# Kernel optimization log

Hardware: AMD Instinct MI355X
Metric: run time of the kernel (lower is better)

## Reference

```python
import jax, jax.numpy as jnp
import numpy as np

N_NODES = 100000
N_EDGES = 1600000
N_EMBED = 48
N_CONVS = 6
N_GRAPHS = 1000
VOCAB = 100


def setup_inputs() -> dict:
    key = jax.random.key(0)
    ks = jax.random.split(key, 20)
    AtomicNum = jax.random.randint(ks[0], (N_NODES,), 0, VOCAB)
    Edge = jax.random.randint(ks[1], (2, N_EDGES), 0, N_NODES)
    graph_id = jnp.sort(jax.random.randint(ks[2], (N_NODES,), 0, N_GRAPHS))
    s = 1.0 / np.sqrt(N_EMBED)
    def lin(k):
        k1, k2 = jax.random.split(k)
        w = jax.random.uniform(k1, (N_EMBED, N_EMBED), jnp.float32, -s, s)
        b = jax.random.uniform(k2, (N_EMBED,), jnp.float32, -s, s)
        return w, b
    def stacked(k):
        ws, bs = zip(*[lin(kk) for kk in jax.random.split(k, N_CONVS)])
        return jnp.stack(ws), jnp.stack(bs)
    emb = jax.random.normal(ks[3], (VOCAB, N_EMBED), jnp.float32)
    msg_w1, msg_b1 = stacked(ks[4])
    msg_w2, msg_b2 = stacked(ks[5])
    upd_w1, upd_b1 = stacked(ks[6])
    upd_w2, upd_b2 = stacked(ks[7])
    ro_w1, ro_b1 = lin(ks[8])
    k1, k2 = jax.random.split(ks[9])
    ro_w2 = jax.random.uniform(k1, (N_EMBED, 1), jnp.float32, -s, s)
    ro_b2 = jax.random.uniform(k2, (1,), jnp.float32, -s, s)
    return dict(AtomicNum=AtomicNum, Edge=Edge, graph_id=graph_id, emb=emb,
                msg_w1=msg_w1, msg_b1=msg_b1, msg_w2=msg_w2, msg_b2=msg_b2,
                upd_w1=upd_w1, upd_b1=upd_b1, upd_w2=upd_w2, upd_b2=upd_b2,
                ro_w1=ro_w1, ro_b1=ro_b1, ro_w2=ro_w2, ro_b2=ro_b2)


def reference(AtomicNum, Edge, graph_id, emb,
              msg_w1, msg_b1, msg_w2, msg_b2,
              upd_w1, upd_b1, upd_w2, upd_b2,
              ro_w1, ro_b1, ro_w2, ro_b2):
    n_nodes = AtomicNum.shape[0]
    src, dst = Edge[0], Edge[1]
    h = emb[AtomicNum]  # [N, d]
    for l in range(N_CONVS):
        # gather endpoint features, elementwise product, message MLP
        x = h[src] * h[dst]                                      # [E, d]
        m = jax.nn.relu(x @ msg_w1[l] + msg_b1[l]) @ msg_w2[l] + msg_b2[l]
        agg = jax.ops.segment_sum(m, dst, num_segments=n_nodes)  # scatter_add
        u = jax.nn.relu(agg @ upd_w1[l] + upd_b1[l]) @ upd_w2[l] + upd_b2[l]
        h = h + u  # residual update
    y = jax.nn.relu(h @ ro_w1 + ro_b1) @ ro_w2 + ro_b2           # [N, 1]
    # per-graph sum readout (== torch.split by Natom + sum per chunk)
    out = jax.ops.segment_sum(y[:, 0], graph_id, num_segments=N_GRAPHS)
    return out
```

## Files before the change

### kernel.cpp

```cpp
#include <hip/hip_runtime.h>
#include <hip/hip_bf16.h>


#define NE 48
#define NB_SH 8
#define SLDS_CAP 1024

typedef __attribute__((ext_vector_type(8))) short short8;
typedef __attribute__((ext_vector_type(4))) float floatx4;

__device__ __forceinline__ unsigned short bf16_rne(float v) {
    unsigned u = __float_as_uint(v);
    u += 0x7FFFu + ((u >> 16) & 1u);
    return (unsigned short)(u >> 16);
}

__device__ __forceinline__ void split8p(const float* __restrict__ x, short8& hi, short8& lo) {
    union { unsigned u[4]; short8 s; } H, L;
#pragma unroll
    for (int i = 0; i < 4; ++i) {
        float a = x[2 * i], b = x[2 * i + 1];
        __hip_bfloat162 h2 = __float22bfloat162_rn(make_float2(a, b));
        unsigned h = *reinterpret_cast<unsigned*>(&h2);
        float ra = a - __uint_as_float(h << 16);
        float rb = b - __uint_as_float(h & 0xFFFF0000u);
        __hip_bfloat162 l2 = __float22bfloat162_rn(make_float2(ra, rb));
        H.u[i] = h;
        L.u[i] = *reinterpret_cast<unsigned*>(&l2);
    }
    hi = H.s; lo = L.s;
}

__device__ __forceinline__ short8 cvt8(const float* __restrict__ x) {
    union { unsigned u[4]; short8 s; } H;
#pragma unroll
    for (int i = 0; i < 4; ++i) {
        __hip_bfloat162 h2 = __float22bfloat162_rn(make_float2(x[2 * i], x[2 * i + 1]));
        H.u[i] = *reinterpret_cast<unsigned*>(&h2);
    }
    return H.s;
}

__device__ __forceinline__ void gemm3(const short8& ah0, const short8& al0,
                                      const short8& ah1, const short8& al1,
                                      const short8* __restrict__ hi,
                                      const short8* __restrict__ lo,
                                      int lane, floatx4* acc) {
#pragma unroll
    for (int t = 0; t < 3; ++t) {
        short8 bh0 = hi[(t * 2 + 0) * 64 + lane];
        short8 bh1 = hi[(t * 2 + 1) * 64 + lane];
        short8 bl0 = lo[(t * 2 + 0) * 64 + lane];
        short8 bl1 = lo[(t * 2 + 1) * 64 + lane];
        floatx4 c = {0.0f, 0.0f, 0.0f, 0.0f};
        c = __builtin_amdgcn_mfma_f32_16x16x32_bf16(ah0, bh0, c, 0, 0, 0);
        c = __builtin_amdgcn_mfma_f32_16x16x32_bf16(ah1, bh1, c, 0, 0, 0);
        c = __builtin_amdgcn_mfma_f32_16x16x32_bf16(al0, bh0, c, 0, 0, 0);
        c = __builtin_amdgcn_mfma_f32_16x16x32_bf16(al1, bh1, c, 0, 0, 0);
        c = __builtin_amdgcn_mfma_f32_16x16x32_bf16(ah0, bl0, c, 0, 0, 0);
        c = __builtin_amdgcn_mfma_f32_16x16x32_bf16(ah1, bl1, c, 0, 0, 0);
        acc[t] = c;
    }
}

__global__ __launch_bounds__(256) void embed_kernel(const int* __restrict__ an,
                                                    const float* __restrict__ emb,
                                                    float* __restrict__ h, int n4) {
    int i = blockIdx.x * 256 + threadIdx.x;
    if (i >= n4) return;
    int n = i / 12, q = i - n * 12;
    ((float4*)h)[i] = ((const float4*)emb)[an[n] * 12 + q];
}

__global__ __launch_bounds__(256) void fold_kernel(const float* __restrict__ w2,
                                                   const float* __restrict__ u1,
                                                   const float* __restrict__ b2,
                                                   float* __restrict__ F,
                                                   float* __restrict__ b2u1) {
    int idx = blockIdx.x * 256 + threadIdx.x;
    if (idx < 6 * NE * NE) {
        int l = idx / (NE * NE);
        int r = idx - l * NE * NE;
        int k = r / NE, j = r - (r / NE) * NE;
        const float* wrow = w2 + (size_t)l * NE * NE + k * NE;
        const float* ucol = u1 + (size_t)l * NE * NE + j;
        float s = 0.0f;
#pragma unroll 8
        for (int q = 0; q < NE; ++q) s = fmaf(wrow[q], ucol[q * NE], s);
        F[idx] = s;
    } else if (idx < 6 * NE * NE + 6 * NE) {
        int r = idx - 6 * NE * NE;
        int l = r / NE, j = r - l * NE;
        const float* bv = b2 + (size_t)l * NE;
        const float* ucol = u1 + (size_t)l * NE * NE + j;
        float s = 0.0f;
#pragma unroll 8
        for (int q = 0; q < NE; ++q) s = fmaf(bv[q], ucol[q * NE], s);
        b2u1[r] = s;
    }
}

__global__ __launch_bounds__(256) void hist_kernel(const int* __restrict__ dst,
                                                   int* __restrict__ cnt, int E) {
    int e = blockIdx.x * 256 + threadIdx.x;
    if (e < E) atomicAdd(&cnt[dst[e]], 1);
}

__global__ __launch_bounds__(256) void scansum_kernel(const int* __restrict__ cnt,
                                                      int* __restrict__ bsum, int N) {
    __shared__ int sw[4];
    const int tid = threadIdx.x, lane = tid & 63, wid = tid >> 6;
    int base = blockIdx.x * 1024;
    int v = 0;
#pragma unroll
    for (int k = 0; k < 4; ++k) {
        int i = base + k * 256 + tid;
        v += (i < N) ? cnt[i] : 0;
    }
#pragma unroll
    for (int o = 1; o < 64; o <<= 1) v += __shfl_xor(v, o, 64);
    if (lane == 0) sw[wid] = v;
    __syncthreads();
    if (tid == 0) bsum[blockIdx.x] = sw[0] + sw[1] + sw[2] + sw[3];
}

__global__ __launch_bounds__(256) void scanb_kernel(int* __restrict__ bsum, int nblk) {
    __shared__ int s[256];
    int tid = threadIdx.x;
    s[tid] = (tid < nblk) ? bsum[tid] : 0;
    __syncthreads();
    if (tid == 0) {
        int run = 0;
        for (int i = 0; i < nblk; ++i) { int t = s[i]; s[i] = run; run += t; }
    }
    __syncthreads();
    if (tid < nblk) bsum[tid] = s[tid];
}

__global__ __launch_bounds__(1024) void scanfix_kernel(const int* __restrict__ cnt,
                                                       const int* __restrict__ bsum,
                                                       int* __restrict__ offs,
                                                       int* __restrict__ gpos, int N) {
    __shared__ int swave[16];
    const int tid = threadIdx.x, lane = tid & 63, wid = tid >> 6;
    int i = blockIdx.x * 1024 + tid;
    int orig = (i < N) ? cnt[i] : 0;
    int v = orig;
#pragma unroll
    for (int off = 1; off < 64; off <<= 1) {
        int u = __shfl_up(v, off, 64);
        if (lane >= off) v += u;
    }
    if (lane == 63) swave[wid] = v;
    __syncthreads();
    if (wid == 0) {
        int w = (lane < 16) ? swave[lane] : 0;
#pragma unroll
        for (int off = 1; off < 16; off <<= 1) {
            int u = __shfl_up(w, off, 64);
            if (lane >= off) w += u;
        }
        if (lane < 16) swave[lane] = w;
    }
    __syncthreads();
    int prefix = (wid > 0) ? swave[wid - 1] : 0;
    int val = bsum[blockIdx.x] + prefix + v - orig;
    if (i < N) {
        offs[i] = val;
        if ((i & 255) == 0) gpos[i >> 8] = val;
    }
}

__global__ __launch_bounds__(256) void partA_kernel(const int* __restrict__ src,
                                                    const int* __restrict__ dst,
                                                    int* __restrict__ gpos,
                                                    int2* __restrict__ pairbuf,
                                                    int E, int NB) {
    __shared__ int lhist[512];
    __shared__ int lbase[512];
    const int tid = threadIdx.x;
    for (int i = tid; i < NB; i += 256) lhist[i] = 0;
    __syncthreads();
    const int base = blockIdx.x * 2048;
    int ssrc[8], sdst[8], rnk[8];
#pragma unroll
    for (int k = 0; k < 8; ++k) {
        int e = base + k * 256 + tid;
        if (e < E) {
            ssrc[k] = src[e]; sdst[k] = dst[e];
            rnk[k] = atomicAdd(&lhist[sdst[k] >> NB_SH], 1);
        }
    }
    __syncthreads();
    for (int i = tid; i < NB; i += 256) {
        int c = lhist[i];
        lbase[i] = c ? atomicAdd(&gpos[i], c) : 0;
    }
    __syncthreads();
#pragma unroll
    for (int k = 0; k < 8; ++k) {
        int e = base + k * 256 + tid;
        if (e < E)
            pairbuf[lbase[sdst[k] >> NB_SH] + rnk[k]] = make_int2(ssrc[k], sdst[k]);
    }
}

__global__ __launch_bounds__(256) void partB_kernel(const int2* __restrict__ pairbuf,
                                                    int* __restrict__ offs,
                                                    int* __restrict__ colsrc, int E) {
    int e = blockIdx.x * 256 + threadIdx.x;
    if (e < E) {
        int2 p = pairbuf[e];
        int pos = atomicAdd(&offs[p.y], 1);
        colsrc[pos] = p.x;
    }
}

__global__ __launch_bounds__(256) void pack_all_kernel(const float* __restrict__ w0,
                                                       const float* __restrict__ w1m,
                                                       const float* __restrict__ w2m,
                                                       const float* __restrict__ w3m,
                                                       short8* __restrict__ hi,
                                                       short8* __restrict__ lo) {
    int idx = blockIdx.x * 256 + threadIdx.x;
    if (idx >= 3 * 2304 + 384) return;
    int slot = idx / 2304;
    int rem  = idx - slot * 2304;
    const float* w = (slot == 0) ? w0 : (slot == 1) ? w1m : (slot == 2) ? w2m : w3m;
    int lane = rem & 63;
    int s = (rem >> 6) & 1;
    int t = (rem >> 7) % 3;
    int l = (rem >> 7) / 3;
    short8 h8, l8;
#pragma unroll
    for (int i = 0; i < 8; ++i) {
        int k = s * 32 + (lane >> 4) * 8 + i;
        int j = t * 16 + (lane & 15);
        float v = (k < NE) ? w[l * NE * NE + k * NE + j] : 0.0f;
        unsigned short hh = bf16_rne(v);
        float hf = __uint_as_float((unsigned)hh << 16);
        unsigned short ll = bf16_rne(v - hf);
        h8[i] = (short)hh;
        l8[i] = (short)ll;
    }
    hi[idx] = h8;
    lo[idx] = l8;
}

__global__ __launch_bounds__(64, 4) void layer_kernel(
    const float* __restrict__ hin,
    const int* __restrict__ colsrc,
    const int* __restrict__ ends,
    const int* __restrict__ cnt,
    float* __restrict__ hout,
    const short8* __restrict__ bhi,
    const short8* __restrict__ blo,
    const float* __restrict__ b1,
    const short8* __restrict__ f1hi, const short8* __restrict__ f1lo,
    const float* __restrict__ b2u1v,
    const float* __restrict__ ub1,
    const short8* __restrict__ u2hi, const short8* __restrict__ u2lo,
    const float* __restrict__ ub2,
    int N,
    int final_layer,
    const int* __restrict__ gid,
    const short8* __restrict__ rw1hi, const short8* __restrict__ rw1lo,
    const float* __restrict__ rb1, const float* __restrict__ rw2,
    const float* __restrict__ rb2, float* __restrict__ out)
{
    __shared__ float mytile[16][52];
    __shared__ float hdls[16][48];
    __shared__ int   slds[SLDS_CAP];
    const int lane = threadIdx.x;
    const int n0   = blockIdx.x * 16;
    if (n0 >= N) return;

    const int m  = lane & 15;
    const int kb = lane >> 4;

    {
        const float4* sp = (const float4*)(hin + (size_t)n0 * NE);
        float4* dp = (float4*)hdls;
#pragma unroll
        for (int f = 0; f < 3; ++f) dp[lane + f * 64] = sp[lane + f * 64];
    }

    const int mydeg = cnt[n0 + m];
    const int myend = ends[n0 + m];

    const int beg0 = __shfl(myend - mydeg, 0, 64);
    const int endL = __shfl(myend, 15, 64);
    const int tot  = endL - beg0;
    const bool uselds = (tot <= SLDS_CAP);
    if (uselds) {
        for (int i = lane; i < tot; i += 64) slds[i] = colsrc[beg0 + i];
    }

    short8 bh[6];
#pragma unroll
    for (int i = 0; i < 6; ++i) bh[i] = bhi[i * 64 + lane];
    const float bb0 = b1[m], bb1 = b1[16 + m], bb2 = b1[32 + m];
    const float rbb0 = fmaxf(bb0, 0.0f), rbb1 = fmaxf(bb1, 0.0f), rbb2 = fmaxf(bb2, 0.0f);
    const float rbb_mine = (lane < 16) ? rbb0 : (lane < 32) ? rbb1 : rbb2;

    asm volatile("s_waitcnt vmcnt(0) lgkmcnt(0)" ::: "memory");

#pragma unroll 1
    for (int nn = 0; nn < 16; ++nn) {
        const int deg = __shfl(mydeg, nn, 64);
        const int end = __shfl(myend, nn, 64);
        const int beg = end - deg;

        const float* hr = hdls[nn];
        float4 d0a = *(const float4*)(hr + kb * 8);
        float4 d0b = *(const float4*)(hr + kb * 8 + 4);
        float4 d1a = make_float4(0, 0, 0, 0), d1b = d1a;
        if (kb < 2) {
            d1a = *(const float4*)(hr + 32 + kb * 8);
            d1b = *(const float4*)(hr + 32 + kb * 8 + 4);
        }

        float s0 = 0.0f, s1 = 0.0f, s2 = 0.0f;
        const int ntile = (deg + 15) >> 4;

        for (int it = 0; it < ntile; ++it) {
            const int rem = deg - it * 16;
            int srow;
            if (uselds) srow = (m < rem) ? slds[beg - beg0 + it * 16 + m] : N;
            else        srow = (m < rem) ? colsrc[beg + it * 16 + m] : N;
            const float* hs = hin + (size_t)srow * NE + kb * 8;

            float x0[8], x1[8];
            {
                float4 a0 = ((const float4*)hs)[0];
                float4 a1 = ((const float4*)hs)[1];
                x0[0] = a0.x * d0a.x; x0[1] = a0.y * d0a.y; x0[2] = a0.z * d0a.z; x0[3] = a0.w * d0a.w;
                x0[4] = a1.x * d0b.x; x0[5] = a1.y * d0b.y; x0[6] = a1.z * d0b.z; x0[7] = a1.w * d0b.w;
            }
            if (kb < 2) {
                float4 a0 = ((const float4*)(hs + 32))[0];
                float4 a1 = ((const float4*)(hs + 32))[1];
                x1[0] = a0.x * d1a.x; x1[1] = a0.y * d1a.y; x1[2] = a0.z * d1a.z; x1[3] = a0.w * d1a.w;
                x1[4] = a1.x * d1b.x; x1[5] = a1.y * d1b.y; x1[6] = a1.z * d1b.z; x1[7] = a1.w * d1b.w;
            } else {
#pragma unroll
                for (int i = 0; i < 8; ++i) x1[i] = 0.0f;
            }

            short8 ah0 = cvt8(x0);
            short8 ah1 = cvt8(x1);

#pragma unroll
            for (int t = 0; t < 3; ++t) {
                floatx4 cc = {0.0f, 0.0f, 0.0f, 0.0f};
                cc = __builtin_amdgcn_mfma_f32_16x16x32_bf16(ah0, bh[t * 2 + 0], cc, 0, 0, 0);
                cc = __builtin_amdgcn_mfma_f32_16x16x32_bf16(ah1, bh[t * 2 + 1], cc, 0, 0, 0);
                const float bb = (t == 0) ? bb0 : (t == 1) ? bb1 : bb2;
                float ts = 0.0f;
#pragma unroll
                for (int r = 0; r < 4; ++r)
                    ts += fmaxf(cc[r] + bb, 0.0f);
                if (t == 0) s0 += ts; else if (t == 1) s1 += ts; else s2 += ts;
            }
        }

        s0 += __shfl_xor(s0, 16, 64); s0 += __shfl_xor(s0, 32, 64);
        s1 += __shfl_xor(s1, 16, 64); s1 += __shfl_xor(s1, 32, 64);
        s2 += __shfl_xor(s2, 16, 64); s2 += __shfl_xor(s2, 32, 64);

        float t1v = __shfl(s1, lane & 15, 64);
        float t2v = __shfl(s2, lane & 15, 64);
        float val = (lane < 16) ? s0 : (lane < 32) ? t1v : t2v;
        const float npad = (float)(ntile * 16 - deg);
        val = fmaf(-npad, rbb_mine, val);
        if (lane < 48) mytile[nn][lane] = val;
    }
    asm volatile("s_waitcnt lgkmcnt(0)" ::: "memory");

    float c0[8], c1[8];
    {
        const float* row = &mytile[m][0];
        *(float4*)(c0)     = *(const float4*)(row + kb * 8);
        *(float4*)(c0 + 4) = *(const float4*)(row + kb * 8 + 4);
        if (kb < 2) {
            *(float4*)(c1)     = *(const float4*)(row + 32 + kb * 8);
            *(float4*)(c1 + 4) = *(const float4*)(row + 32 + kb * 8 + 4);
        } else {
#pragma unroll
            for (int i = 0; i < 8; ++i) c1[i] = 0.0f;
        }
    }
    asm volatile("s_waitcnt lgkmcnt(0)" ::: "memory");
    short8 ah0, al0, ah1, al1;
    split8p(c0, ah0, al0);
    split8p(c1, ah1, al1);

    floatx4 acc[3];
    gemm3(ah0, al0, ah1, al1, f1hi, f1lo, lane, acc);
    {
        float dj[3], bj[3];
#pragma unroll
        for (int t = 0; t < 3; ++t) { dj[t] = b2u1v[t * 16 + m]; bj[t] = ub1[t * 16 + m]; }
#pragma unroll
        for (int r = 0; r < 4; ++r) {
            float fd = (float)__shfl(mydeg, kb * 4 + r, 64);
#pragma unroll
            for (int t = 0; t < 3; ++t)
                acc[t][r] = fmaxf(fmaf(fd, dj[t], acc[t][r]) + bj[t], 0.0f);
        }
    }

#pragma unroll
    for (int t = 0; t < 3; ++t)
#pragma unroll
        for (int r = 0; r < 4; ++r)
            mytile[kb * 4 + r][t * 16 + m] = acc[t][r];
    asm volatile("s_waitcnt lgkmcnt(0)" ::: "memory");
    {
        const float* row = &mytile[m][0];
        *(float4*)(c0)     = *(const float4*)(row + kb * 8);
        *(float4*)(c0 + 4) = *(const float4*)(row + kb * 8 + 4);
        if (kb < 2) {
            *(float4*)(c1)     = *(const float4*)(row + 32 + kb * 8);
            *(float4*)(c1 + 4) = *(const float4*)(row + 32 + kb * 8 + 4);
        } else {
#pragma unroll
            for (int i = 0; i < 8; ++i) c1[i] = 0.0f;
        }
    }
    asm volatile("s_waitcnt lgkmcnt(0)" ::: "memory");
    split8p(c0, ah0, al0);
    split8p(c1, ah1, al1);
    gemm3(ah0, al0, ah1, al1, u2hi, u2lo, lane, acc);

    {
        float bj[3];
#pragma unroll
        for (int t = 0; t < 3; ++t) bj[t] = ub2[t * 16 + m];
#pragma unroll
        for (int r = 0; r < 4; ++r) {
#pragma unroll
            for (int t = 0; t < 3; ++t)
                acc[t][r] += hdls[kb * 4 + r][t * 16 + m] + bj[t];
        }
    }

    if (!final_layer) {
#pragma unroll
        for (int r = 0; r < 4; ++r) {
            const size_t row = (size_t)(n0 + kb * 4 + r) * NE;
#pragma unroll
            for (int t = 0; t < 3; ++t)
                hout[row + t * 16 + m] = acc[t][r];
        }
        return;
    }

#pragma unroll
    for (int t = 0; t < 3; ++t)
#pragma unroll
        for (int r = 0; r < 4; ++r)
            mytile[kb * 4 + r][t * 16 + m] = acc[t][r];
    asm volatile("s_waitcnt lgkmcnt(0)" ::: "memory");
    {
        const float* row = &mytile[m][0];
        *(float4*)(c0)     = *(const float4*)(row + kb * 8);
        *(float4*)(c0 + 4) = *(const float4*)(row + kb * 8 + 4);
        if (kb < 2) {
            *(float4*)(c1)     = *(const float4*)(row + 32 + kb * 8);
            *(float4*)(c1 + 4) = *(const float4*)(row + 32 + kb * 8 + 4);
        } else {
#pragma unroll
            for (int i = 0; i < 8; ++i) c1[i] = 0.0f;
        }
    }
    split8p(c0, ah0, al0);
    split8p(c1, ah1, al1);
    gemm3(ah0, al0, ah1, al1, rw1hi, rw1lo, lane, acc);

    float p[4] = {0.0f, 0.0f, 0.0f, 0.0f};
    {
        float bj[3], wj[3];
#pragma unroll
        for (int t = 0; t < 3; ++t) { bj[t] = rb1[t * 16 + m]; wj[t] = rw2[t * 16 + m]; }
#pragma unroll
        for (int t = 0; t < 3; ++t)
#pragma unroll
            for (int r = 0; r < 4; ++r)
                p[r] = fmaf(fmaxf(acc[t][r] + bj[t], 0.0f), wj[t], p[r]);
    }
#pragma unroll
    for (int o = 1; o < 16; o <<= 1) {
#pragma unroll
        for (int r = 0; r < 4; ++r) p[r] += __shfl_xor(p[r], o, 16);
    }
    if (m == 0) {
        float b2v = rb2[0];
#pragma unroll
        for (int r = 0; r < 4; ++r) {
            int n = n0 + kb * 4 + r;
            atomicAdd(out + gid[n], p[r] + b2v);
        }
    }
}

extern "C" void kernel_launch(void* const* d_in, const int* in_sizes, int n_in,
                              void* d_out, int out_size, void* d_ws, size_t ws_size,
                              hipStream_t stream) {
    const int*   AtomicNum = (const int*)  d_in[0];
    const int*   Edge      = (const int*)  d_in[1];
    const int*   graph_id  = (const int*)  d_in[2];
    const float* emb       = (const float*)d_in[3];
    const float* msg_w1    = (const float*)d_in[4];
    const float* msg_b1    = (const float*)d_in[5];
    const float* msg_w2    = (const float*)d_in[6];
    const float* msg_b2    = (const float*)d_in[7];
    const float* upd_w1    = (const float*)d_in[8];
    const float* upd_b1    = (const float*)d_in[9];
    const float* upd_w2    = (const float*)d_in[10];
    const float* upd_b2    = (const float*)d_in[11];
    const float* ro_w1     = (const float*)d_in[12];
    const float* ro_b1     = (const float*)d_in[13];
    const float* ro_w2     = (const float*)d_in[14];
    const float* ro_b2     = (const float*)d_in[15];

    const int N = in_sizes[0];
    const int E = in_sizes[1] / 2;
    const int* src = Edge;
    const int* dst = Edge + E;
    const int NB = (N + 255) >> NB_SH;
    const int NBLK = (N + 1023) / 1024;

    float*  h    = (float*)d_ws;
    float*  h2   = h  + (size_t)(N + 1) * NE;
    int*    cnt  = (int*)(h2 + (size_t)(N + 1) * NE);
    int*    offs = cnt + N;
    int*    colsrc = offs + N;
    short8* whi  = (short8*)(colsrc + E);
    short8* wlo  = whi + (3 * 2304 + 384);
    int*    gpos = (int*)(wlo + (3 * 2304 + 384));
    int*    bsum = gpos + NB;
    float*  foldF = (float*)(bsum + NBLK);
    float*  b2u1  = foldF + 6 * NE * NE;
    int2*   pairbuf = (int2*)h2;

    hipMemsetAsync(d_out, 0, (size_t)out_size * sizeof(float), stream);
    hipMemsetAsync(cnt, 0, (size_t)N * sizeof(int), stream);
    hipMemsetAsync(h  + (size_t)N * NE, 0, NE * sizeof(float), stream);
    hipMemsetAsync(h2 + (size_t)N * NE, 0, NE * sizeof(float), stream);

    int n4 = N * 12;
    embed_kernel<<<(n4 + 255) / 256, 256, 0, stream>>>(AtomicNum, emb, h, n4);

    fold_kernel<<<(6 * NE * NE + 6 * NE + 255) / 256, 256, 0, stream>>>(
        msg_w2, upd_w1, msg_b2, foldF, b2u1);

    hist_kernel<<<(E + 255) / 256, 256, 0, stream>>>(dst, cnt, E);
    scansum_kernel<<<NBLK, 256, 0, stream>>>(cnt, bsum, N);
    scanb_kernel<<<1, 256, 0, stream>>>(bsum, NBLK);
    scanfix_kernel<<<NBLK, 1024, 0, stream>>>(cnt, bsum, offs, gpos, N);
    partA_kernel<<<(E + 2047) / 2048, 256, 0, stream>>>(src, dst, gpos, pairbuf, E, NB);
    partB_kernel<<<(E + 255) / 256, 256, 0, stream>>>(pairbuf, offs, colsrc, E);

    pack_all_kernel<<<(3 * 2304 + 384 + 255) / 256, 256, 0, stream>>>(
        msg_w1, foldF, upd_w2, ro_w1, whi, wlo);

    const float* hin = h;
    float* hout = h2;
    for (int l = 0; l < 6; ++l) {
        layer_kernel<<<N / 16, 64, 0, stream>>>(
            hin, colsrc, offs, cnt, hout,
            whi + 0 * 2304 + (size_t)l * 384, wlo + 0 * 2304 + (size_t)l * 384,
            msg_b1 + (size_t)l * NE,
            whi + 1 * 2304 + (size_t)l * 384, wlo + 1 * 2304 + (size_t)l * 384,
            b2u1 + (size_t)l * NE,
            upd_b1 + (size_t)l * NE,
            whi + 2 * 2304 + (size_t)l * 384, wlo + 2 * 2304 + (size_t)l * 384,
            upd_b2 + (size_t)l * NE,
            N,
            (l == 5) ? 1 : 0,
            graph_id,
            whi + 3 * 2304, wlo + 3 * 2304,
            ro_b1, ro_w2, ro_b2, (float*)d_out);
        const float* tmp = hin; hin = hout; hout = (float*)tmp;
    }
}
```

Measured before the change: 701.6 us.

## Prefetch gathered source rows into LDS with a flattened multi-stage tile pipeline

```diff
diff --git a/kernel.cpp b/kernel.cpp
--- a/kernel.cpp
+++ b/kernel.cpp
@@ -4,7 +4,9 @@
 
 #define NE 48
 #define NB_SH 8
-#define SLDS_CAP 1024
+#define SLDS_CAP 512
+#define TLIST_CAP 64
+#define PD 3
 
 typedef __attribute__((ext_vector_type(8))) short short8;
 typedef __attribute__((ext_vector_type(4))) float floatx4;
@@ -39,6 +41,12 @@
         H.u[i] = *reinterpret_cast<unsigned*>(&h2);
     }
     return H.s;
+}
+
+__device__ __forceinline__ void gl_lds16(const float* g, float* l) {
+    __builtin_amdgcn_global_load_lds(
+        (const __attribute__((address_space(1))) void*)g,
+        (__attribute__((address_space(3))) void*)l, 16, 0, 0);
 }
 
 __device__ __forceinline__ void gemm3(const short8& ah0, const short8& al0,
@@ -271,6 +279,9 @@
     __shared__ float mytile[16][52];
     __shared__ float hdls[16][48];
     __shared__ int   slds[SLDS_CAP];
+    __shared__ int   tlist[TLIST_CAP];
+    __shared__ float xst[PD][768];
+
     const int lane = threadIdx.x;
     const int n0   = blockIdx.x * 16;
     if (n0 >= N) return;
@@ -296,6 +307,27 @@
         for (int i = lane; i < tot; i += 64) slds[i] = colsrc[beg0 + i];
     }
 
+    int ttot = 0;
+    if (uselds) {
+        const int ntile_m = (mydeg + 15) >> 4;
+        int pref = ntile_m;
+#pragma unroll
+        for (int o = 1; o < 16; o <<= 1) {
+            int u = __shfl_up(pref, o, 64);
+            if ((lane & 15) >= o) pref += u;
+        }
+        ttot = __shfl(pref, 15, 64);
+        if (lane < 16) {
+            const int tstart = pref - ntile_m;
+            const int begrel = (myend - mydeg) - beg0;
+            for (int it = 0; it < ntile_m; ++it) {
+                int rem = mydeg - it * 16;
+                int remc = rem < 16 ? rem : 16;
+                tlist[tstart + it] = (lane << 16) | (remc << 11) | (begrel + it * 16);
+            }
+        }
+    }
+
     short8 bh[6];
 #pragma unroll
     for (int i = 0; i < 6; ++i) bh[i] = bhi[i * 64 + lane];
@@ -303,77 +335,170 @@
     const float rbb0 = fmaxf(bb0, 0.0f), rbb1 = fmaxf(bb1, 0.0f), rbb2 = fmaxf(bb2, 0.0f);
     const float rbb_mine = (lane < 16) ? rbb0 : (lane < 32) ? rbb1 : rbb2;
 
+    {
+        float4 z = make_float4(0, 0, 0, 0);
+        float4* zp = (float4*)&mytile[lane >> 2][(lane & 3) * 12];
+        zp[0] = z; zp[1] = z; zp[2] = z;
+    }
     asm volatile("s_waitcnt vmcnt(0) lgkmcnt(0)" ::: "memory");
 
-#pragma unroll 1
-    for (int nn = 0; nn < 16; ++nn) {
-        const int deg = __shfl(mydeg, nn, 64);
-        const int end = __shfl(myend, nn, 64);
-        const int beg = end - deg;
-
-        const float* hr = hdls[nn];
-        float4 d0a = *(const float4*)(hr + kb * 8);
-        float4 d0b = *(const float4*)(hr + kb * 8 + 4);
-        float4 d1a = make_float4(0, 0, 0, 0), d1b = d1a;
-        if (kb < 2) {
-            d1a = *(const float4*)(hr + 32 + kb * 8);
-            d1b = *(const float4*)(hr + 32 + kb * 8 + 4);
-        }
-
-        float s0 = 0.0f, s1 = 0.0f, s2 = 0.0f;
-        const int ntile = (deg + 15) >> 4;
-
-        for (int it = 0; it < ntile; ++it) {
-            const int rem = deg - it * 16;
-            int srow;
-            if (uselds) srow = (m < rem) ? slds[beg - beg0 + it * 16 + m] : N;
-            else        srow = (m < rem) ? colsrc[beg + it * 16 + m] : N;
-            const float* hs = hin + (size_t)srow * NE + kb * 8;
-
-            float x0[8], x1[8];
-            {
-                float4 a0 = ((const float4*)hs)[0];
-                float4 a1 = ((const float4*)hs)[1];
-                x0[0] = a0.x * d0a.x; x0[1] = a0.y * d0a.y; x0[2] = a0.z * d0a.z; x0[3] = a0.w * d0a.w;
-                x0[4] = a1.x * d0b.x; x0[5] = a1.y * d0b.y; x0[6] = a1.z * d0b.z; x0[7] = a1.w * d0b.w;
-            }
-            if (kb < 2) {
-                float4 a0 = ((const float4*)(hs + 32))[0];
-                float4 a1 = ((const float4*)(hs + 32))[1];
-                x1[0] = a0.x * d1a.x; x1[1] = a0.y * d1a.y; x1[2] = a0.z * d1a.z; x1[3] = a0.w * d1a.w;
-                x1[4] = a1.x * d1b.x; x1[5] = a1.y * d1b.y; x1[6] = a1.z * d1b.z; x1[7] = a1.w * d1b.w;
-            } else {
-#pragma unroll
-                for (int i = 0; i < 8; ++i) x1[i] = 0.0f;
-            }
-
-            short8 ah0 = cvt8(x0);
-            short8 ah1 = cvt8(x1);
-
-#pragma unroll
-            for (int t = 0; t < 3; ++t) {
-                floatx4 cc = {0.0f, 0.0f, 0.0f, 0.0f};
-                cc = __builtin_amdgcn_mfma_f32_16x16x32_bf16(ah0, bh[t * 2 + 0], cc, 0, 0, 0);
-                cc = __builtin_amdgcn_mfma_f32_16x16x32_bf16(ah1, bh[t * 2 + 1], cc, 0, 0, 0);
-                const float bb = (t == 0) ? bb0 : (t == 1) ? bb1 : bb2;
-                float ts = 0.0f;
-#pragma unroll
-                for (int r = 0; r < 4; ++r)
-                    ts += fmaxf(cc[r] + bb, 0.0f);
-                if (t == 0) s0 += ts; else if (t == 1) s1 += ts; else s2 += ts;
-            }
-        }
-
+    float s0 = 0.0f, s1 = 0.0f, s2 = 0.0f;
+    auto finalize = [&](int nn) {
         s0 += __shfl_xor(s0, 16, 64); s0 += __shfl_xor(s0, 32, 64);
         s1 += __shfl_xor(s1, 16, 64); s1 += __shfl_xor(s1, 32, 64);
         s2 += __shfl_xor(s2, 16, 64); s2 += __shfl_xor(s2, 32, 64);
-
         float t1v = __shfl(s1, lane & 15, 64);
         float t2v = __shfl(s2, lane & 15, 64);
         float val = (lane < 16) ? s0 : (lane < 32) ? t1v : t2v;
-        const float npad = (float)(ntile * 16 - deg);
+        int deg = __shfl(mydeg, nn, 64);
+        float npad = (float)((((deg + 15) >> 4) << 4) - deg);
         val = fmaf(-npad, rbb_mine, val);
         if (lane < 48) mytile[nn][lane] = val;
+    };
+
+    if (uselds) {
+        const int r_iss = lane & 15, cg_iss = lane >> 4;
+        auto issue_tile = [&](int ent, int slot, bool dummy) {
+            int srow;
+            if (dummy) {
+                srow = N;
+            } else {
+                int eoff = ent & 2047;
+                int remc = (ent >> 11) & 31;
+                int sr = slds[eoff + r_iss];
+                srow = (r_iss < remc) ? sr : N;
+            }
+            const float* gp = hin + (size_t)srow * NE + cg_iss * 4;
+            float* lb = &xst[slot][0];
+            gl_lds16(gp,      lb);
+            gl_lds16(gp + 16, lb + 256);
+            gl_lds16(gp + 32, lb + 512);
+        };
+
+        if (ttot > 0) {
+#pragma unroll
+            for (int i = 0; i < PD; ++i) {
+                bool real = i < ttot;
+                issue_tile(real ? tlist[i] : 0, i, !real);
+            }
+
+            int curn = -1;
+            float4 d0a = make_float4(0,0,0,0), d0b = d0a, d1a = d0a, d1b = d0a;
+            int slot = 0;
+#pragma unroll 1
+            for (int t = 0; t < ttot; ++t) {
+                int ent = tlist[t];
+                int nn = ent >> 16;
+                if (nn != curn) {
+                    if (curn >= 0) finalize(curn);
+                    curn = nn; s0 = s1 = s2 = 0.0f;
+                    const float* hr = hdls[nn];
+                    d0a = *(const float4*)(hr + kb * 8);
+                    d0b = *(const float4*)(hr + kb * 8 + 4);
+                    if (kb < 2) {
+                        d1a = *(const float4*)(hr + 32 + kb * 8);
+                        d1b = *(const float4*)(hr + 32 + kb * 8 + 4);
+                    }
+                }
+
+                asm volatile("s_waitcnt vmcnt(6)" ::: "memory");
+                __builtin_amdgcn_sched_barrier(0);
+
+                const float* xb = &xst[slot][0];
+                const int o0 = (kb >> 1) * 256 + (kb & 1) * 128 + m * 4;
+                float4 a0 = *(const float4*)(xb + o0);
+                float4 a1 = *(const float4*)(xb + o0 + 64);
+                float x0[8], x1[8];
+                x0[0] = a0.x * d0a.x; x0[1] = a0.y * d0a.y; x0[2] = a0.z * d0a.z; x0[3] = a0.w * d0a.w;
+                x0[4] = a1.x * d0b.x; x0[5] = a1.y * d0b.y; x0[6] = a1.z * d0b.z; x0[7] = a1.w * d0b.w;
+                if (kb < 2) {
+                    const int o2 = 512 + kb * 128 + m * 4;
+                    float4 a2 = *(const float4*)(xb + o2);
+                    float4 a3 = *(const float4*)(xb + o2 + 64);
+                    x1[0] = a2.x * d1a.x; x1[1] = a2.y * d1a.y; x1[2] = a2.z * d1a.z; x1[3] = a2.w * d1a.w;
+                    x1[4] = a3.x * d1b.x; x1[5] = a3.y * d1b.y; x1[6] = a3.z * d1b.z; x1[7] = a3.w * d1b.w;
+                } else {
+#pragma unroll
+                    for (int i = 0; i < 8; ++i) x1[i] = 0.0f;
+                }
+
+                short8 ah0 = cvt8(x0);
+                short8 ah1 = cvt8(x1);
+#pragma unroll
+                for (int tt = 0; tt < 3; ++tt) {
+                    floatx4 cc = {0.0f, 0.0f, 0.0f, 0.0f};
+                    cc = __builtin_amdgcn_mfma_f32_16x16x32_bf16(ah0, bh[tt * 2 + 0], cc, 0, 0, 0);
+                    cc = __builtin_amdgcn_mfma_f32_16x16x32_bf16(ah1, bh[tt * 2 + 1], cc, 0, 0, 0);
+                    const float bb = (tt == 0) ? bb0 : (tt == 1) ? bb1 : bb2;
+                    float ts = 0.0f;
+#pragma unroll
+                    for (int r = 0; r < 4; ++r)
+                        ts += fmaxf(cc[r] + bb, 0.0f);
+                    if (tt == 0) s0 += ts; else if (tt == 1) s1 += ts; else s2 += ts;
+                }
+
+                __builtin_amdgcn_sched_barrier(0);
+                int t2 = t + PD;
+                bool real = t2 < ttot;
+                issue_tile(real ? tlist[t2] : 0, slot, !real);
+                slot = (slot == PD - 1) ? 0 : slot + 1;
+            }
+            if (curn >= 0) finalize(curn);
+            asm volatile("s_waitcnt vmcnt(0)" ::: "memory");
+        }
+    } else {
+#pragma unroll 1
+        for (int nn = 0; nn < 16; ++nn) {
+            const int deg = __shfl(mydeg, nn, 64);
+            const int end = __shfl(myend, nn, 64);
+            const int beg = end - deg;
+            const float* hr = hdls[nn];
+            float4 d0a = *(const float4*)(hr + kb * 8);
+            float4 d0b = *(const float4*)(hr + kb * 8 + 4);
+            float4 d1a = make_float4(0, 0, 0, 0), d1b = d1a;
+            if (kb < 2) {
+                d1a = *(const float4*)(hr + 32 + kb * 8);
+                d1b = *(const float4*)(hr + 32 + kb * 8 + 4);
+            }
+            s0 = s1 = s2 = 0.0f;
+            const int ntile = (deg + 15) >> 4;
+            for (int it = 0; it < ntile; ++it) {
+                const int rem = deg - it * 16;
+                int srow = (m < rem) ? colsrc[beg + it * 16 + m] : N;
+                const float* hs = hin + (size_t)srow * NE + kb * 8;
+                float x0[8], x1[8];
+                {
+                    float4 a0 = ((const float4*)hs)[0];
+                    float4 a1 = ((const float4*)hs)[1];
+                    x0[0] = a0.x * d0a.x; x0[1] = a0.y * d0a.y; x0[2] = a0.z * d0a.z; x0[3] = a0.w * d0a.w;
+                    x0[4] = a1.x * d0b.x; x0[5] = a1.y * d0b.y; x0[6] = a1.z * d0b.z; x0[7] = a1.w * d0b.w;
+                }
+                if (kb < 2) {
+                    float4 a0 = ((const float4*)(hs + 32))[0];
+                    float4 a1 = ((const float4*)(hs + 32))[1];
+                    x1[0] = a0.x * d1a.x; x1[1] = a0.y * d1a.y; x1[2] = a0.z * d1a.z; x1[3] = a0.w * d1a.w;
+                    x1[4] = a1.x * d1b.x; x1[5] = a1.y * d1b.y; x1[6] = a1.z * d1b.z; x1[7] = a1.w * d1b.w;
+                } else {
+#pragma unroll
+                    for (int i = 0; i < 8; ++i) x1[i] = 0.0f;
+                }
+                short8 ah0 = cvt8(x0);
+                short8 ah1 = cvt8(x1);
+#pragma unroll
+                for (int tt = 0; tt < 3; ++tt) {
+                    floatx4 cc = {0.0f, 0.0f, 0.0f, 0.0f};
+                    cc = __builtin_amdgcn_mfma_f32_16x16x32_bf16(ah0, bh[tt * 2 + 0], cc, 0, 0, 0);
+                    cc = __builtin_amdgcn_mfma_f32_16x16x32_bf16(ah1, bh[tt * 2 + 1], cc, 0, 0, 0);
+                    const float bb = (tt == 0) ? bb0 : (tt == 1) ? bb1 : bb2;
+                    float ts = 0.0f;
+#pragma unroll
+                    for (int r = 0; r < 4; ++r)
+                        ts += fmaxf(cc[r] + bb, 0.0f);
+                    if (tt == 0) s0 += ts; else if (tt == 1) s1 += ts; else s2 += ts;
+                }
+            }
+            finalize(nn);
+        }
     }
     asm volatile("s_waitcnt lgkmcnt(0)" ::: "memory");
 
```

Result: slower. 764.4 us (+9.0%).
